# Kernel tuning notes

Measured on AMD Instinct MI355X. Metric: run time of the kernel, lower is better.

The kernel has to match this reference:

```python
import jax, jax.numpy as jnp
import numpy as np

TAKE = 64
HID = 64


def setup_inputs() -> dict:
    key = jax.random.key(0)
    ks = jax.random.split(key, 12)
    B, N, C = 32, 1000, 1601
    s = 1.0 / np.sqrt(C)
    s2 = 1.0 / np.sqrt(HID)
    return {
        "class_logits": jax.random.normal(ks[0], (B, N, C), dtype=jnp.float32),
        "proposals": jax.random.uniform(ks[1], (B, N, 4), dtype=jnp.float32),
        # subject projection (Linear stored as [in, out] so y = x @ W + b)
        "Ws1": jax.random.uniform(ks[2], (C, HID), minval=-s, maxval=s),
        "bs1": jax.random.uniform(ks[3], (HID,), minval=-s, maxval=s),
        "Ws2": jax.random.uniform(ks[4], (HID, HID), minval=-s2, maxval=s2),
        "bs2": jax.random.uniform(ks[5], (HID,), minval=-s2, maxval=s2),
        # object projection
        "Wo1": jax.random.uniform(ks[6], (C, HID), minval=-s, maxval=s),
        "bo1": jax.random.uniform(ks[7], (HID,), minval=-s, maxval=s),
        "Wo2": jax.random.uniform(ks[8], (HID, HID), minval=-s2, maxval=s2),
        "bo2": jax.random.uniform(ks[9], (HID,), minval=-s2, maxval=s2),
    }


def _mlp(x, W1, b1, W2, b2):
    # Linear -> ReLU -> Linear
    return jnp.maximum(x @ W1 + b1, 0.0) @ W2 + b2


def reference(class_logits, proposals, Ws1, bs1, Ws2, bs2, Wo1, bo1, Wo2, bo2):
    B, N, _ = class_logits.shape
    subj = _mlp(class_logits, Ws1, bs1, Ws2, bs2)  # [B, N, 64]
    obj = _mlp(class_logits, Wo1, bo1, Wo2, bo2)   # [B, N, 64]
    # relatedness[b, i, j] = sigmoid(<subj_i, obj_j>)
    scores = jax.nn.sigmoid(jnp.einsum("bnd,bmd->bnm", subj, obj))  # [B, N, N]
    flat = scores.reshape(B, N * N)
    top_scores, top_idx = jax.lax.top_k(flat, TAKE)  # descending, same as sort[:take]
    # flat index k = subject*N + object (row-major), matching the torch meshgrid
    pairs = jnp.stack([top_idx // N, top_idx % N], axis=-1)  # [B, 64, 2] (subj, obj)
    return pairs, top_scores
```

## Files before the change

kernel.cpp:

```cpp
#include <hip/hip_runtime.h>
#include <cstdint>

#define NB 32
#define NN 1000
#define NC 1601
#define HID 64
#define ROWS (NB*NN)
#define CAPB 15360
#define SROWS 15
#define NBIN 4096
#define KCH 32
#define XSTR 68
#define SSTR 132

__device__ __forceinline__ uint32_t f2key(float f){
  uint32_t u = __float_as_uint(f);
  return (u & 0x80000000u) ? ~u : (u | 0x80000000u);
}
__device__ __forceinline__ float key2f(uint32_t k){
  uint32_t u = (k & 0x80000000u) ? (k & 0x7fffffffu) : ~k;
  return __uint_as_float(u);
}

__global__ __launch_bounds__(256, 2) void mlp_kernel(
    const float* __restrict__ x,
    const float* __restrict__ Ws1, const float* __restrict__ bs1,
    const float* __restrict__ Ws2, const float* __restrict__ bs2,
    const float* __restrict__ Wo1, const float* __restrict__ bo1,
    const float* __restrict__ Wo2, const float* __restrict__ bo2,
    float* __restrict__ subj, float* __restrict__ obj)
{
  __shared__ float smem[2*KCH*XSTR];
  __shared__ float xtail[64];
  const int tid = threadIdx.x;
  const int tx  = tid & 15;
  const int ty  = tid >> 4;
  const int row0 = blockIdx.x * 64;

  float accS[4][4], accO[4][4];
  #pragma unroll
  for (int r=0;r<4;r++)
    #pragma unroll
    for (int c=0;c<4;c++){ accS[r][c]=0.f; accO[r][c]=0.f; }

  float stg[8];
  #pragma unroll
  for (int it=0; it<8; it++){
    int u = tid + it*256;
    stg[it] = x[(size_t)(row0 + (u>>5))*NC + (u&31)];
  }

  const int NCHUNK = 50;
  for (int c = 0; c < NCHUNK; c++){
    float* xT = smem + (c & 1)*(KCH*XSTR);
    #pragma unroll
    for (int it=0; it<8; it++){
      int u = tid + it*256;
      xT[(u&31)*XSTR + (u>>5)] = stg[it];
    }
    __syncthreads();
    if (c+1 < NCHUNK){
      const int k0n = (c+1)*KCH;
      #pragma unroll
      for (int it=0; it<8; it++){
        int u = tid + it*256;
        stg[it] = x[(size_t)(row0 + (u>>5))*NC + k0n + (u&31)];
      }
    }
    const float* wS = Ws1 + (size_t)(c*KCH)*HID + tx*4;
    const float* wO = Wo1 + (size_t)(c*KCH)*HID + tx*4;
    #pragma unroll 4
    for (int k=0; k<KCH; k++){
      float4 a  = *(const float4*)&xT[k*XSTR + ty*4];
      float4 bS = *(const float4*)(wS + k*HID);
      float4 bO = *(const float4*)(wO + k*HID);
      float av[4] = {a.x,a.y,a.z,a.w};
      float bs[4] = {bS.x,bS.y,bS.z,bS.w};
      float bo[4] = {bO.x,bO.y,bO.z,bO.w};
      #pragma unroll
      for (int r=0;r<4;r++)
        #pragma unroll
        for (int c2=0;c2<4;c2++){
          accS[r][c2] = fmaf(av[r], bs[c2], accS[r][c2]);
          accO[r][c2] = fmaf(av[r], bo[c2], accO[r][c2]);
        }
    }
  }

  if (tid < 64) xtail[tid] = x[(size_t)(row0 + tid)*NC + 1600];
  __syncthreads();
  {
    float4 a  = *(const float4*)&xtail[ty*4];
    float4 bS = *(const float4*)(Ws1 + (size_t)1600*HID + tx*4);
    float4 bO = *(const float4*)(Wo1 + (size_t)1600*HID + tx*4);
    float av[4] = {a.x,a.y,a.z,a.w};
    float bs[4] = {bS.x,bS.y,bS.z,bS.w};
    float bo[4] = {bO.x,bO.y,bO.z,bO.w};
    #pragma unroll
    for (int r=0;r<4;r++)
      #pragma unroll
      for (int c2=0;c2<4;c2++){
        accS[r][c2] = fmaf(av[r], bs[c2], accS[r][c2]);
        accO[r][c2] = fmaf(av[r], bo[c2], accO[r][c2]);
      }
  }

  float* hT = smem;
  #pragma unroll 1
  for (int head = 0; head < 2; head++){
    const float* b1 = head ? bo1 : bs1;
    const float* b2 = head ? bo2 : bs2;
    const float* W2 = head ? Wo2 : Ws2;
    float* yout     = head ? obj : subj;
    __syncthreads();
    #pragma unroll
    for (int jj=0; jj<4; jj++){
      float bias = b1[tx*4 + jj];
      float4 hv;
      hv.x = fmaxf((head ? accO[0][jj] : accS[0][jj]) + bias, 0.f);
      hv.y = fmaxf((head ? accO[1][jj] : accS[1][jj]) + bias, 0.f);
      hv.z = fmaxf((head ? accO[2][jj] : accS[2][jj]) + bias, 0.f);
      hv.w = fmaxf((head ? accO[3][jj] : accS[3][jj]) + bias, 0.f);
      *(float4*)&hT[(tx*4+jj)*XSTR + ty*4] = hv;
    }
    __syncthreads();
    float accY[4][4];
    #pragma unroll
    for (int c2=0;c2<4;c2++){
      float bv = b2[tx*4 + c2];
      #pragma unroll
      for (int r=0;r<4;r++) accY[r][c2] = bv;
    }
    #pragma unroll 4
    for (int d=0; d<64; d++){
      float4 a = *(const float4*)&hT[d*XSTR + ty*4];
      float4 w = *(const float4*)(W2 + d*HID + tx*4);
      float av[4] = {a.x,a.y,a.z,a.w};
      float wv[4] = {w.x,w.y,w.z,w.w};
      #pragma unroll
      for (int r=0;r<4;r++)
        #pragma unroll
        for (int c2=0;c2<4;c2++)
          accY[r][c2] = fmaf(av[r], wv[c2], accY[r][c2]);
    }
    #pragma unroll
    for (int r=0;r<4;r++)
      *(float4*)&yout[(size_t)(row0 + ty*4 + r)*HID + tx*4] =
        make_float4(accY[r][0], accY[r][1], accY[r][2], accY[r][3]);
  }
}

__global__ __launch_bounds__(1024, 4) void sample_thresh(
    const float* __restrict__ subj, const float* __restrict__ obj,
    uint32_t* __restrict__ L)
{
  __shared__ float sRows[SROWS*HID];
  __shared__ uint32_t keys[SROWS*NN];
  __shared__ uint32_t hist[256];
  __shared__ uint32_t sb[2];
  const int b = blockIdx.x, tid = threadIdx.x;

  const float4* sp = (const float4*)(subj + (size_t)b*NN*HID);
  if (tid < SROWS*16) ((float4*)sRows)[tid] = sp[tid];
  __syncthreads();

  for (int j = tid; j < NN; j += 1024){
    const float4* op4 = (const float4*)(obj + ((size_t)b*NN + j)*HID);
    float4 o[16];
    #pragma unroll
    for (int q=0;q<16;q++) o[q] = op4[q];
    #pragma unroll 1
    for (int i=0;i<SROWS;i++){
      const float4* s4 = (const float4*)(sRows + i*HID);
      float acc = 0.f;
      #pragma unroll
      for (int q=0;q<16;q++){
        float4 s = s4[q];
        acc = fmaf(s.x, o[q].x, acc); acc = fmaf(s.y, o[q].y, acc);
        acc = fmaf(s.z, o[q].z, acc); acc = fmaf(s.w, o[q].w, acc);
      }
      keys[i*NN + j] = f2key(acc);
    }
  }
  __syncthreads();

  uint32_t prefix = 0; int remaining = 64;
  for (int round = 0; round < 2; round++){
    const int shift = 24 - round*8;
    if (tid < 256) hist[tid] = 0;
    __syncthreads();
    for (int idx = tid; idx < SROWS*NN; idx += 1024){
      uint32_t k = keys[idx];
      bool match = (round == 0) || ((k >> 24) == (prefix >> 24));
      if (match) atomicAdd(&hist[(k >> shift) & 255u], 1u);
    }
    __syncthreads();
    if (tid == 0){
      uint32_t cum = 0; int bin = 255;
      for (;; bin--){ cum += hist[bin]; if (cum >= (uint32_t)remaining || bin == 0) break; }
      sb[0] = (uint32_t)bin;
      sb[1] = (uint32_t)(remaining - (int)(cum - hist[bin]));
    }
    __syncthreads();
    prefix |= sb[0] << shift;
    remaining = (int)sb[1];
    __syncthreads();
  }
  if (tid == 0) L[b] = prefix;
}

__device__ __forceinline__ void score_tile_acc(
    const float* __restrict__ subj, const float* __restrict__ obj,
    int b, int ti, int tj, int tid,
    float* __restrict__ sT, float* __restrict__ oT, float (&acc)[8][8])
{
  const int tx = tid & 15, ty = tid >> 4;
  #pragma unroll
  for (int a=0;a<8;a++)
    #pragma unroll
    for (int c=0;c<8;c++) acc[a][c] = 0.f;

  #pragma unroll 1
  for (int half = 0; half < 2; half++){
    __syncthreads();
    {
      const float4* gp = (const float4*)subj;
      #pragma unroll
      for (int it=0; it<4; it++){
        int u = tid + it*256;
        int r = u >> 3, q = (u & 7) + half*8;
        int gr = b*NN + ti + r; gr = gr < ROWS ? gr : (ROWS-1);
        float4 v = gp[(size_t)gr*16 + q];
        int kk = (u & 7)*4;
        sT[(kk+0)*SSTR + r] = v.x;
        sT[(kk+1)*SSTR + r] = v.y;
        sT[(kk+2)*SSTR + r] = v.z;
        sT[(kk+3)*SSTR + r] = v.w;
      }
      const float4* gp2 = (const float4*)obj;
      #pragma unroll
      for (int it=0; it<4; it++){
        int u = tid + it*256;
        int r = u >> 3, q = (u & 7) + half*8;
        int gr = b*NN + tj + r; gr = gr < ROWS ? gr : (ROWS-1);
        float4 v = gp2[(size_t)gr*16 + q];
        int kk = (u & 7)*4;
        oT[(kk+0)*SSTR + r] = v.x;
        oT[(kk+1)*SSTR + r] = v.y;
        oT[(kk+2)*SSTR + r] = v.z;
        oT[(kk+3)*SSTR + r] = v.w;
      }
    }
    __syncthreads();
    #pragma unroll 2
    for (int k=0; k<32; k++){
      float4 s0 = *(const float4*)&sT[k*SSTR + ty*8];
      float4 s1 = *(const float4*)&sT[k*SSTR + ty*8 + 4];
      float4 o0 = *(const float4*)&oT[k*SSTR + tx*8];
      float4 o1 = *(const float4*)&oT[k*SSTR + tx*8 + 4];
      float s[8] = {s0.x,s0.y,s0.z,s0.w,s1.x,s1.y,s1.z,s1.w};
      float o[8] = {o0.x,o0.y,o0.z,o0.w,o1.x,o1.y,o1.z,o1.w};
      #pragma unroll
      for (int a=0;a<8;a++)
        #pragma unroll
        for (int c=0;c<8;c++)
          acc[a][c] = fmaf(s[a], o[c], acc[a][c]);
    }
  }
}

__global__ __launch_bounds__(256, 3) void score_pass1(
    const float* __restrict__ subj, const float* __restrict__ obj,
    const uint32_t* __restrict__ L, uint32_t* __restrict__ cnt,
    uint2* __restrict__ cand, uint32_t* __restrict__ ghist)
{
  __shared__ float sT[32*SSTR];
  __shared__ float oT[32*SSTR];
  __shared__ uint32_t hist[NBIN];
  __shared__ uint32_t lcnt, gbase;
  const int blk = blockIdx.x;
  const int b   = blk >> 6;
  const int t   = blk & 63;
  const int ti  = (t >> 3) << 7;
  const int tj  = (t & 7)  << 7;
  const int tid = threadIdx.x;
  const int tx = tid & 15, ty = tid >> 4;

  for (int i = tid; i < NBIN; i += 256) hist[i] = 0;
  if (tid == 0) lcnt = 0;

  float acc[8][8];
  score_tile_acc(subj, obj, b, ti, tj, tid, sT, oT, acc);

  const uint32_t Lb = L[b];
  int myCnt = 0;
  #pragma unroll
  for (int a=0;a<8;a++){
    int gi = ti + ty*8 + a;
    #pragma unroll
    for (int c=0;c<8;c++){
      int gj = tj + tx*8 + c;
      if (gi < NN && gj < NN){
        uint32_t key = f2key(acc[a][c]);
        if (key >= Lb){ myCnt++; atomicAdd(&hist[key >> 20], 1u); }
      }
    }
  }
  uint32_t lbase = atomicAdd(&lcnt, (uint32_t)myCnt);
  __syncthreads();
  if (tid == 0) gbase = atomicAdd(&cnt[b], lcnt);
  __syncthreads();
  uint32_t pos = gbase + lbase;
  #pragma unroll
  for (int a=0;a<8;a++){
    int gi = ti + ty*8 + a;
    #pragma unroll
    for (int c=0;c<8;c++){
      int gj = tj + tx*8 + c;
      if (gi < NN && gj < NN){
        uint32_t key = f2key(acc[a][c]);
        if (key >= Lb){
          if (pos < CAPB) cand[(size_t)b*CAPB + pos] = make_uint2(key, (uint32_t)(gi*NN + gj));
          pos++;
        }
      }
    }
  }
  __syncthreads();
  for (int i = tid; i < NBIN; i += 256){
    uint32_t v = hist[i];
    if (v) atomicAdd(&ghist[(size_t)b*NBIN + i], v);
  }
}

__global__ __launch_bounds__(256, 1) void pick_thresh(
    const uint32_t* __restrict__ ghist, const uint32_t* __restrict__ cnt,
    uint32_t* __restrict__ T, uint32_t* __restrict__ flag)
{
  __shared__ uint32_t S[256];
  const int b = blockIdx.x, tid = threadIdx.x;
  const uint32_t* h = ghist + (size_t)b*NBIN;
  uint32_t loc[16];
  uint32_t s = 0;
  #pragma unroll
  for (int i=0;i<16;i++){ loc[i] = h[tid*16 + i]; s += loc[i]; }
  S[tid] = s;
  __syncthreads();
  for (int off = 1; off < 256; off <<= 1){
    uint32_t v = (tid + off < 256) ? S[tid + off] : 0u;
    __syncthreads();
    S[tid] += v;
    __syncthreads();
  }
  uint32_t above = (tid < 255) ? S[tid + 1] : 0u;
  if (above < 64u && S[tid] >= 64u){
    uint32_t suf = above; int best = 0;
    for (int i=15;i>=0;i--){ suf += loc[i]; if (suf >= 64u){ best = i; break; } }
    T[b] = (uint32_t)(tid*16 + best) << 20;
  }
  if (tid == 0) flag[b] = (cnt[b] > (uint32_t)CAPB) ? 1u : 0u;
}

__global__ __launch_bounds__(256, 3) void score_repair(
    const float* __restrict__ subj, const float* __restrict__ obj,
    const uint32_t* __restrict__ T, const uint32_t* __restrict__ flag,
    uint32_t* __restrict__ cnt2, uint2* __restrict__ cand)
{
  const int blk = blockIdx.x;
  const int b   = blk >> 6;
  if (flag[b] == 0u) return;

  __shared__ float sT[32*SSTR];
  __shared__ float oT[32*SSTR];
  __shared__ uint32_t lcnt, gbase;
  const int t   = blk & 63;
  const int ti  = (t >> 3) << 7;
  const int tj  = (t & 7)  << 7;
  const int tid = threadIdx.x;
  const int tx = tid & 15, ty = tid >> 4;

  if (tid == 0) lcnt = 0;

  float acc[8][8];
  score_tile_acc(subj, obj, b, ti, tj, tid, sT, oT, acc);

  const uint32_t Tb = T[b];
  int myCnt = 0;
  #pragma unroll
  for (int a=0;a<8;a++){
    int gi = ti + ty*8 + a;
    #pragma unroll
    for (int c=0;c<8;c++){
      int gj = tj + tx*8 + c;
      if (gi < NN && gj < NN && f2key(acc[a][c]) >= Tb) myCnt++;
    }
  }
  uint32_t lbase = atomicAdd(&lcnt, (uint32_t)myCnt);
  __syncthreads();
  if (tid == 0) gbase = atomicAdd(&cnt2[b], lcnt);
  __syncthreads();
  uint32_t pos = gbase + lbase;
  #pragma unroll
  for (int a=0;a<8;a++){
    int gi = ti + ty*8 + a;
    #pragma unroll
    for (int c=0;c<8;c++){
      int gj = tj + tx*8 + c;
      if (gi < NN && gj < NN){
        uint32_t key = f2key(acc[a][c]);
        if (key >= Tb){
          if (pos < CAPB) cand[(size_t)b*CAPB + pos] = make_uint2(key, (uint32_t)(gi*NN + gj));
          pos++;
        }
      }
    }
  }
}

__global__ __launch_bounds__(1024, 4) void final_select(
    const uint32_t* __restrict__ cnt, const uint32_t* __restrict__ cnt2,
    const uint32_t* __restrict__ flag, const uint2* __restrict__ cand,
    float* __restrict__ out)
{
  __shared__ uint32_t keys[CAPB];
  __shared__ uint32_t hist[256];
  __shared__ uint32_t sb[2];
  __shared__ uint2 win[192];
  __shared__ uint32_t wn;
  const int b = blockIdx.x, tid = threadIdx.x;
  uint32_t n0 = flag[b] ? cnt2[b] : cnt[b];
  const int n = (n0 < (uint32_t)CAPB) ? (int)n0 : CAPB;

  for (int i = tid; i < n; i += 1024) keys[i] = cand[(size_t)b*CAPB + i].x;
  if (tid == 0) wn = 0;
  __syncthreads();

  uint32_t prefix = 0; int remaining = 64;
  for (int round = 0; round < 4; round++){
    const int shift = 24 - round*8;
    if (tid < 256) hist[tid] = 0;
    __syncthreads();
    for (int i = tid; i < n; i += 1024){
      uint32_t k = keys[i];
      bool match = (round == 0) || ((k >> (shift+8)) == (prefix >> (shift+8)));
      if (match) atomicAdd(&hist[(k >> shift) & 255u], 1u);
    }
    __syncthreads();
    if (tid == 0){
      uint32_t cum = 0; int bin = 255;
      for (;; bin--){ cum += hist[bin]; if (cum >= (uint32_t)remaining || bin == 0) break; }
      sb[0] = (uint32_t)bin;
      sb[1] = (uint32_t)(remaining - (int)(cum - hist[bin]));
    }
    __syncthreads();
    prefix |= sb[0] << shift;
    remaining = (int)sb[1];
    __syncthreads();
  }
  const uint32_t Tk = prefix;

  for (int i = tid; i < n; i += 1024){
    if (keys[i] >= Tk){
      uint32_t p = atomicAdd(&wn, 1u);
      if (p < 192u) win[p] = make_uint2(keys[i], cand[(size_t)b*CAPB + i].y);
    }
  }
  __syncthreads();
  const int m = (wn < 192u) ? (int)wn : 192;

  if (tid < m){
    const uint64_t me = ((uint64_t)win[tid].x << 32) | (uint64_t)(uint32_t)(~win[tid].y);
    int rank = 0;
    for (int s = 0; s < m; s++){
      uint64_t oth = ((uint64_t)win[s].x << 32) | (uint64_t)(uint32_t)(~win[s].y);
      rank += (oth > me) ? 1 : 0;
    }
    if (rank < 64){
      const uint32_t f = win[tid].y;
      const float d  = key2f(win[tid].x);
      const float sc = 1.0f / (1.0f + expf(-d));
      out[((size_t)b*64 + rank)*2 + 0] = (float)(f / NN);
      out[((size_t)b*64 + rank)*2 + 1] = (float)(f % NN);
      out[(size_t)NB*64*2 + (size_t)b*64 + rank] = sc;
    }
  }
}

extern "C" void kernel_launch(void* const* d_in, const int* in_sizes, int n_in,
                              void* d_out, int out_size, void* d_ws, size_t ws_size,
                              hipStream_t stream) {
  const float* x   = (const float*)d_in[0];
  const float* Ws1 = (const float*)d_in[2];
  const float* bs1 = (const float*)d_in[3];
  const float* Ws2 = (const float*)d_in[4];
  const float* bs2 = (const float*)d_in[5];
  const float* Wo1 = (const float*)d_in[6];
  const float* bo1 = (const float*)d_in[7];
  const float* Wo2 = (const float*)d_in[8];
  const float* bo2 = (const float*)d_in[9];
  float* out = (float*)d_out;

  char* ws = (char*)d_ws;
  float*    subj = (float*)ws;
  float*    objp = (float*)(ws + 8192000);
  uint32_t* L    = (uint32_t*)(ws + 16384000);
  uint32_t* cnt  = (uint32_t*)(ws + 16384128);
  uint32_t* cnt2 = (uint32_t*)(ws + 16384256);
  uint32_t* ghist= (uint32_t*)(ws + 16384384);
  uint32_t* T    = (uint32_t*)(ws + 16908672);
  uint32_t* flag = (uint32_t*)(ws + 16908800);
  uint2*    cand = (uint2*)   (ws + 16908928);

  hipMemsetAsync(cnt, 0, 128 + 128 + 524288, stream);

  mlp_kernel<<<ROWS/64, 256, 0, stream>>>(x, Ws1, bs1, Ws2, bs2,
                                          Wo1, bo1, Wo2, bo2, subj, objp);
  sample_thresh<<<NB, 1024, 0, stream>>>(subj, objp, L);
  score_pass1<<<NB*64, 256, 0, stream>>>(subj, objp, L, cnt, cand, ghist);
  pick_thresh<<<NB, 256, 0, stream>>>(ghist, cnt, T, flag);
  score_repair<<<NB*64, 256, 0, stream>>>(subj, objp, T, flag, cnt2, cand);
  final_select<<<NB, 1024, 0, stream>>>(cnt, cnt2, flag, cand, out);
}
```

Measured before the change: 715.5 us.

## Stage first-layer weights in LDS and double per-thread tile in MLP kernel

The MLP kernel now uses 128 threads per 64-row block, with each thread computing an 8x4 tile for both heads instead of 4x4. Each chunk of the Ws1/Wo1 first-layer weights is loaded cooperatively into a double-buffered shared-memory region rather than each thread reading it from global memory. The two second-layer heads are computed together in one pass. This is meant to cut global weight traffic and raise arithmetic intensity per LDS load, at the cost of more registers, more shared memory and fewer threads per block.

```diff
diff --git a/kernel.cpp b/kernel.cpp
--- a/kernel.cpp
+++ b/kernel.cpp
@@ -10,7 +10,10 @@
 #define SROWS 15
 #define NBIN 4096
 #define KCH 32
+#define RB 64
+#define TPB 128
 #define XSTR 68
+#define WSTR 132
 #define SSTR 132
 
 __device__ __forceinline__ uint32_t f2key(float f){
@@ -22,7 +25,7 @@
   return __uint_as_float(u);
 }
 
-__global__ __launch_bounds__(256, 2) void mlp_kernel(
+__global__ __launch_bounds__(TPB, 1) void mlp_kernel(
     const float* __restrict__ x,
     const float* __restrict__ Ws1, const float* __restrict__ bs1,
     const float* __restrict__ Ws2, const float* __restrict__ bs2,
@@ -30,123 +33,164 @@
     const float* __restrict__ Wo2, const float* __restrict__ bo2,
     float* __restrict__ subj, float* __restrict__ obj)
 {
-  __shared__ float smem[2*KCH*XSTR];
-  __shared__ float xtail[64];
+  __shared__ float smem[2*KCH*XSTR + 2*KCH*WSTR];
+  __shared__ float xtail[RB];
   const int tid = threadIdx.x;
   const int tx  = tid & 15;
   const int ty  = tid >> 4;
-  const int row0 = blockIdx.x * 64;
-
-  float accS[4][4], accO[4][4];
-  #pragma unroll
-  for (int r=0;r<4;r++)
+  const int row0 = blockIdx.x * RB;
+
+  float* xbuf = smem;
+  float* wbuf = smem + 2*KCH*XSTR;
+
+  float accS[8][4], accO[8][4];
+  #pragma unroll
+  for (int r=0;r<8;r++)
     #pragma unroll
     for (int c=0;c<4;c++){ accS[r][c]=0.f; accO[r][c]=0.f; }
 
-  float stg[8];
+  float  xstg[16];
+  float4 wstg[8];
+  #pragma unroll
+  for (int it=0; it<16; it++){
+    int u = tid + it*TPB;
+    xstg[it] = x[(size_t)(row0 + (u>>5))*NC + (u&31)];
+  }
   #pragma unroll
   for (int it=0; it<8; it++){
-    int u = tid + it*256;
-    stg[it] = x[(size_t)(row0 + (u>>5))*NC + (u&31)];
+    int u = tid + it*TPB;
+    int k = u>>5, c4 = u&31;
+    const float* src = (c4 < 16) ? (Ws1 + (size_t)k*HID + c4*4)
+                                 : (Wo1 + (size_t)k*HID + (c4-16)*4);
+    wstg[it] = *(const float4*)src;
   }
 
   const int NCHUNK = 50;
   for (int c = 0; c < NCHUNK; c++){
-    float* xT = smem + (c & 1)*(KCH*XSTR);
+    float* xT = xbuf + (c & 1)*(KCH*XSTR);
+    float* wC = wbuf + (c & 1)*(KCH*WSTR);
+    #pragma unroll
+    for (int it=0; it<16; it++){
+      int u = tid + it*TPB;
+      xT[(u&31)*XSTR + (u>>5)] = xstg[it];
+    }
     #pragma unroll
     for (int it=0; it<8; it++){
-      int u = tid + it*256;
-      xT[(u&31)*XSTR + (u>>5)] = stg[it];
+      int u = tid + it*TPB;
+      *(float4*)&wC[(u>>5)*WSTR + (u&31)*4] = wstg[it];
     }
     __syncthreads();
     if (c+1 < NCHUNK){
       const int k0n = (c+1)*KCH;
       #pragma unroll
+      for (int it=0; it<16; it++){
+        int u = tid + it*TPB;
+        xstg[it] = x[(size_t)(row0 + (u>>5))*NC + k0n + (u&31)];
+      }
+      #pragma unroll
       for (int it=0; it<8; it++){
-        int u = tid + it*256;
-        stg[it] = x[(size_t)(row0 + (u>>5))*NC + k0n + (u&31)];
-      }
-    }
-    const float* wS = Ws1 + (size_t)(c*KCH)*HID + tx*4;
-    const float* wO = Wo1 + (size_t)(c*KCH)*HID + tx*4;
+        int u = tid + it*TPB;
+        int k = u>>5, c4 = u&31;
+        const float* src = (c4 < 16) ? (Ws1 + (size_t)(k0n+k)*HID + c4*4)
+                                     : (Wo1 + (size_t)(k0n+k)*HID + (c4-16)*4);
+        wstg[it] = *(const float4*)src;
+      }
+    }
     #pragma unroll 4
     for (int k=0; k<KCH; k++){
-      float4 a  = *(const float4*)&xT[k*XSTR + ty*4];
-      float4 bS = *(const float4*)(wS + k*HID);
-      float4 bO = *(const float4*)(wO + k*HID);
-      float av[4] = {a.x,a.y,a.z,a.w};
-      float bs[4] = {bS.x,bS.y,bS.z,bS.w};
-      float bo[4] = {bO.x,bO.y,bO.z,bO.w};
-      #pragma unroll
-      for (int r=0;r<4;r++)
+      float4 a0 = *(const float4*)&xT[k*XSTR + ty*8];
+      float4 a1 = *(const float4*)&xT[k*XSTR + ty*8 + 4];
+      float4 bS = *(const float4*)&wC[k*WSTR + tx*4];
+      float4 bO = *(const float4*)&wC[k*WSTR + 64 + tx*4];
+      float av[8] = {a0.x,a0.y,a0.z,a0.w,a1.x,a1.y,a1.z,a1.w};
+      float bs_[4] = {bS.x,bS.y,bS.z,bS.w};
+      float bo_[4] = {bO.x,bO.y,bO.z,bO.w};
+      #pragma unroll
+      for (int r=0;r<8;r++)
         #pragma unroll
         for (int c2=0;c2<4;c2++){
-          accS[r][c2] = fmaf(av[r], bs[c2], accS[r][c2]);
-          accO[r][c2] = fmaf(av[r], bo[c2], accO[r][c2]);
+          accS[r][c2] = fmaf(av[r], bs_[c2], accS[r][c2]);
+          accO[r][c2] = fmaf(av[r], bo_[c2], accO[r][c2]);
         }
     }
   }
 
-  if (tid < 64) xtail[tid] = x[(size_t)(row0 + tid)*NC + 1600];
+  if (tid < RB) xtail[tid] = x[(size_t)(row0 + tid)*NC + 1600];
   __syncthreads();
   {
-    float4 a  = *(const float4*)&xtail[ty*4];
+    float4 a0 = *(const float4*)&xtail[ty*8];
+    float4 a1 = *(const float4*)&xtail[ty*8 + 4];
     float4 bS = *(const float4*)(Ws1 + (size_t)1600*HID + tx*4);
     float4 bO = *(const float4*)(Wo1 + (size_t)1600*HID + tx*4);
-    float av[4] = {a.x,a.y,a.z,a.w};
-    float bs[4] = {bS.x,bS.y,bS.z,bS.w};
-    float bo[4] = {bO.x,bO.y,bO.z,bO.w};
-    #pragma unroll
-    for (int r=0;r<4;r++)
+    float av[8] = {a0.x,a0.y,a0.z,a0.w,a1.x,a1.y,a1.z,a1.w};
+    float bs_[4] = {bS.x,bS.y,bS.z,bS.w};
+    float bo_[4] = {bO.x,bO.y,bO.z,bO.w};
+    #pragma unroll
+    for (int r=0;r<8;r++)
       #pragma unroll
       for (int c2=0;c2<4;c2++){
-        accS[r][c2] = fmaf(av[r], bs[c2], accS[r][c2]);
-        accO[r][c2] = fmaf(av[r], bo[c2], accO[r][c2]);
-      }
-  }
-
-  float* hT = smem;
-  #pragma unroll 1
-  for (int head = 0; head < 2; head++){
-    const float* b1 = head ? bo1 : bs1;
-    const float* b2 = head ? bo2 : bs2;
-    const float* W2 = head ? Wo2 : Ws2;
-    float* yout     = head ? obj : subj;
-    __syncthreads();
-    #pragma unroll
-    for (int jj=0; jj<4; jj++){
-      float bias = b1[tx*4 + jj];
-      float4 hv;
-      hv.x = fmaxf((head ? accO[0][jj] : accS[0][jj]) + bias, 0.f);
-      hv.y = fmaxf((head ? accO[1][jj] : accS[1][jj]) + bias, 0.f);
-      hv.z = fmaxf((head ? accO[2][jj] : accS[2][jj]) + bias, 0.f);
-      hv.w = fmaxf((head ? accO[3][jj] : accS[3][jj]) + bias, 0.f);
-      *(float4*)&hT[(tx*4+jj)*XSTR + ty*4] = hv;
-    }
-    __syncthreads();
-    float accY[4][4];
-    #pragma unroll
-    for (int c2=0;c2<4;c2++){
-      float bv = b2[tx*4 + c2];
-      #pragma unroll
-      for (int r=0;r<4;r++) accY[r][c2] = bv;
-    }
-    #pragma unroll 4
-    for (int d=0; d<64; d++){
-      float4 a = *(const float4*)&hT[d*XSTR + ty*4];
-      float4 w = *(const float4*)(W2 + d*HID + tx*4);
-      float av[4] = {a.x,a.y,a.z,a.w};
-      float wv[4] = {w.x,w.y,w.z,w.w};
-      #pragma unroll
-      for (int r=0;r<4;r++)
-        #pragma unroll
-        for (int c2=0;c2<4;c2++)
-          accY[r][c2] = fmaf(av[r], wv[c2], accY[r][c2]);
-    }
-    #pragma unroll
-    for (int r=0;r<4;r++)
-      *(float4*)&yout[(size_t)(row0 + ty*4 + r)*HID + tx*4] =
-        make_float4(accY[r][0], accY[r][1], accY[r][2], accY[r][3]);
+        accS[r][c2] = fmaf(av[r], bs_[c2], accS[r][c2]);
+        accO[r][c2] = fmaf(av[r], bo_[c2], accO[r][c2]);
+      }
+  }
+
+  float* hTS = smem;
+  float* hTO = smem + 64*XSTR;
+  __syncthreads();
+  #pragma unroll
+  for (int jj=0; jj<4; jj++){
+    float bS = bs1[tx*4 + jj];
+    float bO = bo1[tx*4 + jj];
+    float4 h0, h1;
+    h0.x = fmaxf(accS[0][jj]+bS, 0.f); h0.y = fmaxf(accS[1][jj]+bS, 0.f);
+    h0.z = fmaxf(accS[2][jj]+bS, 0.f); h0.w = fmaxf(accS[3][jj]+bS, 0.f);
+    h1.x = fmaxf(accS[4][jj]+bS, 0.f); h1.y = fmaxf(accS[5][jj]+bS, 0.f);
+    h1.z = fmaxf(accS[6][jj]+bS, 0.f); h1.w = fmaxf(accS[7][jj]+bS, 0.f);
+    *(float4*)&hTS[(tx*4+jj)*XSTR + ty*8]     = h0;
+    *(float4*)&hTS[(tx*4+jj)*XSTR + ty*8 + 4] = h1;
+    h0.x = fmaxf(accO[0][jj]+bO, 0.f); h0.y = fmaxf(accO[1][jj]+bO, 0.f);
+    h0.z = fmaxf(accO[2][jj]+bO, 0.f); h0.w = fmaxf(accO[3][jj]+bO, 0.f);
+    h1.x = fmaxf(accO[4][jj]+bO, 0.f); h1.y = fmaxf(accO[5][jj]+bO, 0.f);
+    h1.z = fmaxf(accO[6][jj]+bO, 0.f); h1.w = fmaxf(accO[7][jj]+bO, 0.f);
+    *(float4*)&hTO[(tx*4+jj)*XSTR + ty*8]     = h0;
+    *(float4*)&hTO[(tx*4+jj)*XSTR + ty*8 + 4] = h1;
+  }
+  __syncthreads();
+
+  float accYS[8][4], accYO[8][4];
+  #pragma unroll
+  for (int c2=0;c2<4;c2++){
+    float bvS = bs2[tx*4 + c2];
+    float bvO = bo2[tx*4 + c2];
+    #pragma unroll
+    for (int r=0;r<8;r++){ accYS[r][c2] = bvS; accYO[r][c2] = bvO; }
+  }
+  #pragma unroll 2
+  for (int d=0; d<64; d++){
+    float4 aS0 = *(const float4*)&hTS[d*XSTR + ty*8];
+    float4 aS1 = *(const float4*)&hTS[d*XSTR + ty*8 + 4];
+    float4 aO0 = *(const float4*)&hTO[d*XSTR + ty*8];
+    float4 aO1 = *(const float4*)&hTO[d*XSTR + ty*8 + 4];
+    float4 wS = *(const float4*)(Ws2 + (size_t)d*HID + tx*4);
+    float4 wO = *(const float4*)(Wo2 + (size_t)d*HID + tx*4);
+    float aS[8] = {aS0.x,aS0.y,aS0.z,aS0.w,aS1.x,aS1.y,aS1.z,aS1.w};
+    float aO[8] = {aO0.x,aO0.y,aO0.z,aO0.w,aO1.x,aO1.y,aO1.z,aO1.w};
+    float wSv[4] = {wS.x,wS.y,wS.z,wS.w};
+    float wOv[4] = {wO.x,wO.y,wO.z,wO.w};
+    #pragma unroll
+    for (int r=0;r<8;r++)
+      #pragma unroll
+      for (int c2=0;c2<4;c2++){
+        accYS[r][c2] = fmaf(aS[r], wSv[c2], accYS[r][c2]);
+        accYO[r][c2] = fmaf(aO[r], wOv[c2], accYO[r][c2]);
+      }
+  }
+  #pragma unroll
+  for (int r=0;r<8;r++){
+    *(float4*)&subj[(size_t)(row0 + ty*8 + r)*HID + tx*4] =
+      make_float4(accYS[r][0], accYS[r][1], accYS[r][2], accYS[r][3]);
+    *(float4*)&obj[(size_t)(row0 + ty*8 + r)*HID + tx*4] =
+      make_float4(accYO[r][0], accYO[r][1], accYO[r][2], accYO[r][3]);
   }
 }
 
@@ -513,7 +557,7 @@
 
   hipMemsetAsync(cnt, 0, 128 + 128 + 524288, stream);
 
-  mlp_kernel<<<ROWS/64, 256, 0, stream>>>(x, Ws1, bs1, Ws2, bs2,
+  mlp_kernel<<<ROWS/RB, TPB, 0, stream>>>(x, Ws1, bs1, Ws2, bs2,
                                           Wo1, bo1, Wo2, bo2, subj, objp);
   sample_thresh<<<NB, 1024, 0, stream>>>(subj, objp, L);
   score_pass1<<<NB*64, 256, 0, stream>>>(subj, objp, L, cnt, cand, ghist);
```

After: 732.2 us. 2.3% more time.
